# Kernel optimization log

Measured on AMD Instinct MI355X. Metric: run time of the kernel, lower is better.

## Reference

```python
import jax, jax.numpy as jnp
import numpy as np

B_BATCH = 16384   # number of independent control queries (timesteps/trials)
P = 32            # observation dim p = C.shape[0]
MC = 16           # control dim m_control = B.shape[1]
H = 24            # h (== h_tilde in the module, since it sets self.h_tilde = h)
M = 64            # m (== m_tilde, since the module sets self.m_tilde = m)
L = M + M + 1     # history length needed: max delay is j+k = m_tilde + m - 1


def setup_inputs() -> dict:
    key = jax.random.key(0)
    ks = jax.random.split(key, 9)
    return {
        # y_rev[b, d, :] == y_nat_history[-d-1] (most-recent-first reversed history)
        "y_rev": jax.random.normal(ks[0], (B_BATCH, L, P), dtype=jnp.float32),
        "M0": jax.random.normal(ks[1], (MC, P), dtype=jnp.float32),
        "M_tilde": jax.random.normal(ks[2], (H, MC, P), dtype=jnp.float32),
        "M_0l": jax.random.normal(ks[3], (H, MC, P), dtype=jnp.float32),
        "M_big": jax.random.normal(ks[4], (H, H, MC, P), dtype=jnp.float32),
        # eigenvalues of the PSD Hankel matrices: positive
        "sigma": jax.random.uniform(ks[5], (H,), dtype=jnp.float32, minval=0.01, maxval=1.0),
        "lambda_e": jax.random.uniform(ks[6], (H,), dtype=jnp.float32, minval=0.01, maxval=1.0),
        "phi": jax.random.normal(ks[7], (M, H), dtype=jnp.float32),
        "phi_tilde": jax.random.normal(ks[8], (M, H), dtype=jnp.float32),
    }


def reference(y_rev, M0, M_tilde, M_0l, M_big, sigma, lambda_e, phi, phi_tilde):
    # Term 1: M_0 @ y_t  -> [B, MC]
    u = jnp.einsum("cp,bp->bc", M0, y_rev[:, 0])

    # Term 2: sum_{i,j>=1} lambda_i^{1/4} phi_tilde[j-1,i] (M_tilde[i] @ y_{t-j})
    pt = phi_tilde * (lambda_e ** 0.25)[None, :]            # [M, H] (j-1, i)
    T2 = jnp.einsum("ji,icp->jcp", pt, M_tilde)             # [M, MC, P]
    u = u + jnp.einsum("jcp,bjp->bc", T2, y_rev[:, 1:M + 1])

    # Term 3: sum_{l,k>=0} sigma_l^{1/4} phi[k,l] (M_0l[l] @ y_{t-k})
    ps = phi * (sigma ** 0.25)[None, :]                     # [M, H] (k, l)
    T3 = jnp.einsum("kl,lcp->kcp", ps, M_0l)                # [M, MC, P]
    u = u + jnp.einsum("kcp,bkp->bc", T3, y_rev[:, 0:M])

    # Term 4: sum_{i,j,l,k} (sigma_l lambda_i)^{1/4} phi[k,l] phi_tilde[j-1,i] (M[i][l] @ y_{t-j-k})
    # Collapse (j,k) into delay d=j+k via 1-D convolution per (i,l):
    #   conv(phi_tilde[:,i], phi[:,l])[n] corresponds to delay d = n+1.
    conv = jax.vmap(jax.vmap(jnp.convolve, in_axes=(None, 1)), in_axes=(1, None))
    W4 = conv(phi_tilde, phi)                               # [H(i), H(l), 2M-1]
    scale = (lambda_e[:, None] * sigma[None, :]) ** 0.25    # [H(i), H(l)]
    T4 = jnp.einsum("ild,ilcp->dcp", W4 * scale[:, :, None], M_big)  # [2M-1, MC, P]
    u = u + jnp.einsum("dcp,bdp->bc", T4, y_rev[:, 1:2 * M])

    return u  # [B, MC]
```

## Files before the change

### kernel.cpp

```cpp
#include <hip/hip_runtime.h>

#define BB    16384
#define PP    32
#define MCC   16
#define HH    24
#define MM    64
#define LL    129
#define YROW  (LL*PP)
#define KK    4096

#define RB    32
#define TPB   512
#define NST   32
#define SK    128
#define BUF4  1024

typedef __attribute__((ext_vector_type(8))) _Float16 half8;
typedef __attribute__((ext_vector_type(4))) float    f32x4;

__device__ __forceinline__ void dma16(const float* g, float4* l) {
    __builtin_amdgcn_global_load_lds(
        (const __attribute__((address_space(1))) void*)g,
        (__attribute__((address_space(3))) void*)l, 16, 0, 0);
}

__global__ __launch_bounds__(256) void setup_k(
    const float* __restrict__ M0,  const float* __restrict__ Mt,
    const float* __restrict__ M0l, const float* __restrict__ Mb,
    const float* __restrict__ sig, const float* __restrict__ lam,
    const float* __restrict__ phi, const float* __restrict__ phit,
    float* __restrict__ Wk)
{
    __shared__ float sA[MM*HH];
    __shared__ float sB[MM*HH];
    __shared__ float sWd[HH*HH];

    const int t = threadIdx.x;
    const int d = blockIdx.x >> 1;
    const int h = blockIdx.x & 1;

#pragma unroll
    for (int r = 0; r < 6; ++r) {
        int e = t + r*256;
        int col = e % HH;
        sA[e] = phit[e] * sqrtf(sqrtf(lam[col]));
        sB[e] = phi[e]  * sqrtf(sqrtf(sig[col]));
    }
    __syncthreads();

    if (d >= 1) {
        const int n  = d - 1;
        const int lo = n > 63 ? n - 63 : 0;
        const int hi = n < 63 ? n : 63;
        for (int e = t; e < HH*HH; e += 256) {
            int i = e / HH, l = e % HH;
            float s = 0.f;
            for (int j = lo; j <= hi; ++j) s += sA[j*HH + i] * sB[(n - j)*HH + l];
            sWd[e] = s;
        }
    }
    __syncthreads();

    const int c = h*8 + (t >> 5);
    const int p = t & 31;
    float wv = 0.f;
    if (d == 0) wv += M0[c*PP + p];
    if (d >= 1 && d <= MM) {
        const int j = d - 1;
#pragma unroll
        for (int i = 0; i < HH; ++i) wv += sA[j*HH + i] * Mt[(i*MCC + c)*PP + p];
    }
    if (d < MM) {
#pragma unroll
        for (int l = 0; l < HH; ++l) wv += sB[d*HH + l] * M0l[(l*MCC + c)*PP + p];
    }
    if (d >= 1) {
        const float* mb = Mb + h*256 + t;
#pragma unroll 16
        for (int e = 0; e < HH*HH; ++e) wv += sWd[e] * mb[e*512];
    }
    Wk[(d*PP + p)*MCC + c] = wv;
}

__global__ __launch_bounds__(512) void pack_k(
    const float* __restrict__ Wk,
    _Float16* __restrict__ Bh, _Float16* __restrict__ Bm, _Float16* __restrict__ Bl)
{
    const int kb = blockIdx.x;
    const int t  = threadIdx.x;
    const int l  = t >> 3, j = t & 7;
    const int k  = kb*32 + (l >> 4)*8 + j;
    const int c  = l & 15;
    const float v = Wk[k*MCC + c];
    const _Float16 h  = (_Float16)v;
    const float    r1 = v - (float)h;
    const _Float16 m  = (_Float16)r1;
    const float    r2 = r1 - (float)m;
    const _Float16 lo = (_Float16)r2;
    const int idx = kb*512 + l*8 + j;
    Bh[idx] = h; Bm[idx] = m; Bl[idx] = lo;
}

__global__ __launch_bounds__(512, 4) void main_k(
    const float* __restrict__ Y,
    const half8* __restrict__ Bh, const half8* __restrict__ Bm,
    const half8* __restrict__ Bl,
    float* __restrict__ out)
{
    __shared__ float4 sY[2*BUF4];

    const int t    = threadIdx.x;
    const int w    = t >> 6;
    const int lane = t & 63;
    const int blk  = blockIdx.x;

    const int r0 = t >> 5;
    const int c4 = t & 31;
    const float* g0 = Y + (size_t)(blk*RB + r0     )*YROW + ((c4 ^ (r0 & 7))*4);
    const float* g1 = Y + (size_t)(blk*RB + r0 + 16)*YROW + ((c4 ^ (r0 & 7))*4);
    float4* const dA0 = &sY[       w*64];
    float4* const dA1 = &sY[512  + w*64];
    float4* const dB0 = &sY[BUF4       + w*64];
    float4* const dB1 = &sY[BUF4 + 512 + w*64];

    const int rt = w & 1;
    const int kh = w >> 1;
    const int rloc = lane & 15;
    const int o    = lane >> 4;
    const int r    = rt*16 + rloc;
    const int rx   = r & 7;
    const int f0   = kh*8 + o*2;
    const int s0   = r*32 + ( f0      ^ rx);
    const int s1   = r*32 + ((f0 + 1) ^ rx);

    f32x4 acc = {0.f, 0.f, 0.f, 0.f};

    dma16(g0, dA0);
    dma16(g1, dA1);

#pragma unroll 1
    for (int s = 0; s < NST; ++s) {
        __syncthreads();

        if (s + 1 < NST) {
            const float* p0 = g0 + (s + 1)*SK;
            const float* p1 = g1 + (s + 1)*SK;
            if ((s + 1) & 1) { dma16(p0, dB0); dma16(p1, dB1); }
            else             { dma16(p0, dA0); dma16(p1, dA1); }
        }

        const float4* yb = &sY[(s & 1) ? BUF4 : 0];
        const float4 y0 = yb[s0];
        const float4 y1 = yb[s1];
        const float ya[8] = {y0.x, y0.y, y0.z, y0.w, y1.x, y1.y, y1.z, y1.w};

        half8 ah, am, al;
#pragma unroll
        for (int j = 0; j < 8; ++j) {
            const float v  = ya[j];
            const _Float16 hh = (_Float16)v;
            const float    q1 = v - (float)hh;
            const _Float16 mm = (_Float16)q1;
            const float    q2 = q1 - (float)mm;
            ah[j] = hh; am[j] = mm; al[j] = (_Float16)q2;
        }

        const int bi = (s*4 + kh)*64 + lane;
        const half8 bh = Bh[bi];
        const half8 bm = Bm[bi];
        const half8 bl = Bl[bi];

        acc = __builtin_amdgcn_mfma_f32_16x16x32_f16(ah, bh, acc, 0, 0, 0);
        acc = __builtin_amdgcn_mfma_f32_16x16x32_f16(ah, bm, acc, 0, 0, 0);
        acc = __builtin_amdgcn_mfma_f32_16x16x32_f16(am, bh, acc, 0, 0, 0);
        acc = __builtin_amdgcn_mfma_f32_16x16x32_f16(ah, bl, acc, 0, 0, 0);
        acc = __builtin_amdgcn_mfma_f32_16x16x32_f16(am, bm, acc, 0, 0, 0);
        acc = __builtin_amdgcn_mfma_f32_16x16x32_f16(al, bh, acc, 0, 0, 0);
    }

    __syncthreads();
    float* red = (float*)sY;
#pragma unroll
    for (int i = 0; i < 4; ++i) red[(w*64 + lane)*4 + i] = acc[i];
    __syncthreads();

    {
        const int orow = t >> 4;
        const int oc   = t & 15;
        const int ort  = orow >> 4, orl = orow & 15;
        const int ol   = (orl >> 2)*16 + oc;
        const int oreg = orl & 3;
        float ssum = 0.f;
#pragma unroll
        for (int q = 0; q < 4; ++q)
            ssum += red[((q*2 + ort)*64 + ol)*4 + oreg];
        out[(size_t)(blk*RB + orow)*MCC + oc] = ssum;
    }
}

extern "C" void kernel_launch(void* const* d_in, const int* in_sizes, int n_in,
                              void* d_out, int out_size, void* d_ws, size_t ws_size,
                              hipStream_t stream) {
    (void)in_sizes; (void)n_in; (void)out_size; (void)ws_size;
    const float* y    = (const float*)d_in[0];
    const float* M0   = (const float*)d_in[1];
    const float* Mt   = (const float*)d_in[2];
    const float* M0l  = (const float*)d_in[3];
    const float* Mb   = (const float*)d_in[4];
    const float* sig  = (const float*)d_in[5];
    const float* lam  = (const float*)d_in[6];
    const float* phi  = (const float*)d_in[7];
    const float* phit = (const float*)d_in[8];

    float*    Wk = (float*)d_ws;
    _Float16* Bh = (_Float16*)(Wk + KK*MCC);
    _Float16* Bm = Bh + KK*MCC;
    _Float16* Bl = Bm + KK*MCC;
    float*   out = (float*)d_out;

    setup_k<<<256, 256, 0, stream>>>(M0, Mt, M0l, Mb, sig, lam, phi, phit, Wk);
    pack_k <<<128, 512, 0, stream>>>(Wk, Bh, Bm, Bl);
    main_k <<<512, TPB, 0, stream>>>(y, (const half8*)Bh, (const half8*)Bm,
                                     (const half8*)Bl, out);
}
```

Measured before the change: 425.7 us.

## Fuse pack into setup and triple-buffer Y loads with prefetched B fragments

Folds the fp16 three-way split and MFMA-layout packing into the setup kernel, removing one launch and the float workspace round trip. The main kernel moves from double to triple-buffered LDS staging of Y, issuing loads two steps ahead, and prefetches the next step's B fragments into registers. The __syncthreads is replaced by explicit vmcnt waits plus s_barrier. This adds LDS use, which may lower occupancy, and the hand-counted vmcnt values must match the number of outstanding loads.

```diff
diff --git a/kernel.cpp b/kernel.cpp
--- a/kernel.cpp
+++ b/kernel.cpp
@@ -29,7 +29,8 @@
     const float* __restrict__ M0l, const float* __restrict__ Mb,
     const float* __restrict__ sig, const float* __restrict__ lam,
     const float* __restrict__ phi, const float* __restrict__ phit,
-    float* __restrict__ Wk)
+    _Float16* __restrict__ Bh, _Float16* __restrict__ Bm,
+    _Float16* __restrict__ Bl)
 {
     __shared__ float sA[MM*HH];
     __shared__ float sB[MM*HH];
@@ -79,35 +80,24 @@
 #pragma unroll 16
         for (int e = 0; e < HH*HH; ++e) wv += sWd[e] * mb[e*512];
     }
-    Wk[(d*PP + p)*MCC + c] = wv;
-}
-
-__global__ __launch_bounds__(512) void pack_k(
-    const float* __restrict__ Wk,
-    _Float16* __restrict__ Bh, _Float16* __restrict__ Bm, _Float16* __restrict__ Bl)
-{
-    const int kb = blockIdx.x;
-    const int t  = threadIdx.x;
-    const int l  = t >> 3, j = t & 7;
-    const int k  = kb*32 + (l >> 4)*8 + j;
-    const int c  = l & 15;
-    const float v = Wk[k*MCC + c];
-    const _Float16 h  = (_Float16)v;
-    const float    r1 = v - (float)h;
-    const _Float16 m  = (_Float16)r1;
-    const float    r2 = r1 - (float)m;
-    const _Float16 lo = (_Float16)r2;
-    const int idx = kb*512 + l*8 + j;
-    Bh[idx] = h; Bm[idx] = m; Bl[idx] = lo;
+
+    const int k   = d*PP + p;
+    const int kb  = k >> 5, q = k & 31;
+    const int idx = kb*512 + ((q >> 3)*16 + c)*8 + (q & 7);
+    const _Float16 hh = (_Float16)wv;
+    const float    r1 = wv - (float)hh;
+    const _Float16 mm = (_Float16)r1;
+    const float    r2 = r1 - (float)mm;
+    Bh[idx] = hh; Bm[idx] = mm; Bl[idx] = (_Float16)r2;
 }
 
 __global__ __launch_bounds__(512, 4) void main_k(
     const float* __restrict__ Y,
-    const half8* __restrict__ Bh, const half8* __restrict__ Bm,
-    const half8* __restrict__ Bl,
+    const half8* __restrict__ Bh8, const half8* __restrict__ Bm8,
+    const half8* __restrict__ Bl8,
     float* __restrict__ out)
 {
-    __shared__ float4 sY[2*BUF4];
+    __shared__ float4 sY[3*BUF4];
 
     const int t    = threadIdx.x;
     const int w    = t >> 6;
@@ -118,10 +108,6 @@
     const int c4 = t & 31;
     const float* g0 = Y + (size_t)(blk*RB + r0     )*YROW + ((c4 ^ (r0 & 7))*4);
     const float* g1 = Y + (size_t)(blk*RB + r0 + 16)*YROW + ((c4 ^ (r0 & 7))*4);
-    float4* const dA0 = &sY[       w*64];
-    float4* const dA1 = &sY[512  + w*64];
-    float4* const dB0 = &sY[BUF4       + w*64];
-    float4* const dB1 = &sY[BUF4 + 512 + w*64];
 
     const int rt = w & 1;
     const int kh = w >> 1;
@@ -133,23 +119,43 @@
     const int s0   = r*32 + ( f0      ^ rx);
     const int s1   = r*32 + ((f0 + 1) ^ rx);
 
+    const half8* bh = Bh8 + kh*64 + lane;
+    const half8* bm = Bm8 + kh*64 + lane;
+    const half8* bl = Bl8 + kh*64 + lane;
+
     f32x4 acc = {0.f, 0.f, 0.f, 0.f};
 
-    dma16(g0, dA0);
-    dma16(g1, dA1);
+    {
+        float4* d0 = &sY[w*64];
+        dma16(g0, d0); dma16(g1, d0 + 512);
+    }
+    half8 cbh = bh[0], cbm = bm[0], cbl = bl[0];
+    {
+        float4* d1 = &sY[BUF4 + w*64];
+        dma16(g0 + SK, d1); dma16(g1 + SK, d1 + 512);
+    }
+    half8 nbh, nbm, nbl;
 
 #pragma unroll 1
     for (int s = 0; s < NST; ++s) {
-        __syncthreads();
-
-        if (s + 1 < NST) {
-            const float* p0 = g0 + (s + 1)*SK;
-            const float* p1 = g1 + (s + 1)*SK;
-            if ((s + 1) & 1) { dma16(p0, dB0); dma16(p1, dB1); }
-            else             { dma16(p0, dA0); dma16(p1, dA1); }
-        }
-
-        const float4* yb = &sY[(s & 1) ? BUF4 : 0];
+        if (s < NST - 1) asm volatile("s_waitcnt vmcnt(5)" ::: "memory");
+        else             asm volatile("s_waitcnt vmcnt(3)" ::: "memory");
+        __builtin_amdgcn_s_barrier();
+        asm volatile("" ::: "memory");
+
+        if (s < NST - 1) {
+            const int bi = (s + 1)*256;
+            nbh = bh[bi]; nbm = bm[bi]; nbl = bl[bi];
+        }
+        asm volatile("" ::: "memory");
+
+        if (s < NST - 2) {
+            float4* dd = &sY[((s + 2) % 3)*BUF4 + w*64];
+            dma16(g0 + (s + 2)*SK, dd); dma16(g1 + (s + 2)*SK, dd + 512);
+        }
+        asm volatile("" ::: "memory");
+
+        const float4* yb = &sY[(s % 3)*BUF4];
         const float4 y0 = yb[s0];
         const float4 y1 = yb[s1];
         const float ya[8] = {y0.x, y0.y, y0.z, y0.w, y1.x, y1.y, y1.z, y1.w};
@@ -165,17 +171,14 @@
             ah[j] = hh; am[j] = mm; al[j] = (_Float16)q2;
         }
 
-        const int bi = (s*4 + kh)*64 + lane;
-        const half8 bh = Bh[bi];
-        const half8 bm = Bm[bi];
-        const half8 bl = Bl[bi];
-
-        acc = __builtin_amdgcn_mfma_f32_16x16x32_f16(ah, bh, acc, 0, 0, 0);
-        acc = __builtin_amdgcn_mfma_f32_16x16x32_f16(ah, bm, acc, 0, 0, 0);
-        acc = __builtin_amdgcn_mfma_f32_16x16x32_f16(am, bh, acc, 0, 0, 0);
-        acc = __builtin_amdgcn_mfma_f32_16x16x32_f16(ah, bl, acc, 0, 0, 0);
-        acc = __builtin_amdgcn_mfma_f32_16x16x32_f16(am, bm, acc, 0, 0, 0);
-        acc = __builtin_amdgcn_mfma_f32_16x16x32_f16(al, bh, acc, 0, 0, 0);
+        acc = __builtin_amdgcn_mfma_f32_16x16x32_f16(ah, cbh, acc, 0, 0, 0);
+        acc = __builtin_amdgcn_mfma_f32_16x16x32_f16(ah, cbm, acc, 0, 0, 0);
+        acc = __builtin_amdgcn_mfma_f32_16x16x32_f16(am, cbh, acc, 0, 0, 0);
+        acc = __builtin_amdgcn_mfma_f32_16x16x32_f16(ah, cbl, acc, 0, 0, 0);
+        acc = __builtin_amdgcn_mfma_f32_16x16x32_f16(am, cbm, acc, 0, 0, 0);
+        acc = __builtin_amdgcn_mfma_f32_16x16x32_f16(al, cbh, acc, 0, 0, 0);
+
+        cbh = nbh; cbm = nbm; cbl = nbl;
     }
 
     __syncthreads();
@@ -212,14 +215,13 @@
     const float* phi  = (const float*)d_in[7];
     const float* phit = (const float*)d_in[8];
 
-    float*    Wk = (float*)d_ws;
-    _Float16* Bh = (_Float16*)(Wk + KK*MCC);
+    _Float16* Bh = (_Float16*)d_ws;
     _Float16* Bm = Bh + KK*MCC;
     _Float16* Bl = Bm + KK*MCC;
     float*   out = (float*)d_out;
 
-    setup_k<<<256, 256, 0, stream>>>(M0, Mt, M0l, Mb, sig, lam, phi, phit, Wk);
-    pack_k <<<128, 512, 0, stream>>>(Wk, Bh, Bm, Bl);
+    setup_k<<<256, 256, 0, stream>>>(M0, Mt, M0l, Mb, sig, lam, phi, phit,
+                                     Bh, Bm, Bl);
     main_k <<<512, TPB, 0, stream>>>(y, (const half8*)Bh, (const half8*)Bm,
                                      (const half8*)Bl, out);
 }
```

After: 419.3 us. About the same (-1.5%).
